# Optimization experiments

Measured on AMD Instinct MI355X. Metric: run time of the kernel, lower is better.

Reference implementation:

```python
import jax, jax.numpy as jnp
import numpy as np

TOP_K = 2

def setup_inputs() -> dict:
    key = jax.random.key(0)
    k1, k2 = jax.random.split(key)
    x = jax.random.normal(k1, (8, 4096, 4096), dtype=jnp.float32)
    # nn.Linear weight [num_experts, dim]
    gate_w = jax.random.normal(k2, (64, 4096), dtype=jnp.float32) * (1.0 / np.sqrt(4096))
    return {"x": x, "gate_w": gate_w}

def reference(x, gate_w):
    # logits: [B, S, E]
    logits = jnp.einsum('bsd,ed->bse', x, gate_w)
    routing_weights = jax.nn.softmax(logits, axis=-1)
    top_weights, top_indices = jax.lax.top_k(routing_weights, TOP_K)
    top_weights = top_weights / jnp.sum(top_weights, axis=-1, keepdims=True)
    return top_weights, top_indices
```

## Files before the change

kernel.cpp:

```cpp
#include <hip/hip_runtime.h>
#include <hip/hip_bf16.h>
#include <math.h>


typedef __attribute__((ext_vector_type(8))) short short8;
typedef __attribute__((ext_vector_type(4))) float f32x4;

#define TPB 64
#define NCH 128
#define TAU 1e-4f
#define LROW 68

__device__ __forceinline__ void cvt8(const f32x4* v, short8* hi, short8* lo) {
    const float* f = reinterpret_cast<const float*>(v);
#pragma unroll
    for (int j = 0; j < 8; ++j) {
        __hip_bfloat16 h = __float2bfloat16(f[j]);
        float r = f[j] - __bfloat162float(h);
        __hip_bfloat16 l = __float2bfloat16(r);
        (*hi)[j] = (short)*reinterpret_cast<unsigned short*>(&h);
        (*lo)[j] = (short)*reinterpret_cast<unsigned short*>(&l);
    }
}

__global__ void prep_b(const float* __restrict__ gw,
                       short8* __restrict__ bh, short8* __restrict__ bl) {
    const int tid = blockIdx.x * 256 + threadIdx.x;
    const int ln  = tid & 63;
    const int w   = (tid >> 6) & 127;
    const int nt  = tid >> 13;
    const int row = nt * 16 + (ln & 15);
    const int k   = w * 32 + ((ln >> 4) << 3);
    f32x4 v[2];
    v[0] = *reinterpret_cast<const f32x4*>(gw + (long)row * 4096 + k);
    v[1] = *reinterpret_cast<const f32x4*>(gw + (long)row * 4096 + k + 4);
    short8 h, l;
    cvt8(v, &h, &l);
    bh[tid] = h;
    bl[tid] = l;
}

__device__ __forceinline__ void gload16(const void* g, void* l) {
    __builtin_amdgcn_global_load_lds(
        (const __attribute__((address_space(1))) void*)g,
        (__attribute__((address_space(3))) void*)l, 16, 0, 0);
}

#define STAGE(C, MBUF) do {                                                   \
    char* aB = AB + (MBUF) * 16384;                                           \
    char* bB = aB + 8192;                                                     \
    _Pragma("unroll")                                                         \
    for (int i = 0; i < 2; ++i)                                               \
        gload16(srcA[i] + (long)(C) * 128, aB + (wv * 2 + i) * 1024 + ln * 16); \
    _Pragma("unroll")                                                         \
    for (int i = 0; i < 2; ++i) {                                             \
        const int s  = wv * 2 + i;                                            \
        const short8* sp = ((s & 1) ? blp : bhp)                              \
            + ((long)(s >> 1) * 8192 + (long)(C) * 64 + ln);                  \
        gload16(sp, bB + s * 1024 + ln * 16);                                 \
    }                                                                         \
} while (0)

__global__ __launch_bounds__(256, 3)
void router_fused(const float* __restrict__ x,
                  const short8* __restrict__ bhp,
                  const short8* __restrict__ blp,
                  const float* __restrict__ gw,
                  float* __restrict__ out,
                  int M, int K) {
    __shared__ __align__(16) char AB[49152];
    __shared__ int flags[TPB];
    __shared__ double Ld4[4][64];

    const int t  = threadIdx.x;
    const int wv = t >> 6;
    const int ln = t & 63;
    const int fr = ln & 15;
    const int q  = ln >> 4;
    const long tok0 = (long)blockIdx.x * TPB;
    const int phase = blockIdx.x & (NCH - 1);

    const char* srcA[2];
#pragma unroll
    for (int i = 0; i < 2; ++i) {
        const int row  = (wv * 2 + i) * 8 + (ln >> 3);
        const int slot = (ln & 7) ^ (row & 7);
        srcA[i] = (const char*)x + (tok0 + row) * (long)K * 4 + slot * 16;
    }

    f32x4 acc[4];
#pragma unroll
    for (int nt = 0; nt < 4; ++nt) acc[nt] = (f32x4){0.f, 0.f, 0.f, 0.f};

    STAGE(phase, 0);
    STAGE((phase + 1) & (NCH - 1), 1);

    const int R  = wv * 16 + fr;
    const int rk = R & 7;

    for (int j = 0; j < NCH; ++j) {
        const int c = (phase + j) & (NCH - 1);
        const int m = j % 3;
        if (j < NCH - 1) asm volatile("s_waitcnt vmcnt(4)" ::: "memory");
        else             asm volatile("s_waitcnt vmcnt(0)" ::: "memory");
        __builtin_amdgcn_s_barrier();
        asm volatile("" ::: "memory");
        if (j + 2 < NCH) STAGE((phase + j + 2) & (NCH - 1), (j + 2) % 3);
        __builtin_amdgcn_sched_barrier(0);

        {
            const char* aB = AB + m * 16384 + R * 128;
            const char* bB = AB + m * 16384 + 8192;
            f32x4 av[2];
            av[0] = *(const f32x4*)(aB + (((q * 2 + 0) ^ rk) * 16));
            av[1] = *(const f32x4*)(aB + (((q * 2 + 1) ^ rk) * 16));
            short8 ah, al;
            cvt8(av, &ah, &al);
            __builtin_amdgcn_s_setprio(1);
#pragma unroll
            for (int nt = 0; nt < 4; ++nt) {
                short8 bhv = *(const short8*)(bB + (nt * 2 + 0) * 1024 + ln * 16);
                short8 blv = *(const short8*)(bB + (nt * 2 + 1) * 1024 + ln * 16);
                acc[nt] = __builtin_amdgcn_mfma_f32_16x16x32_bf16(ah, bhv, acc[nt], 0, 0, 0);
                acc[nt] = __builtin_amdgcn_mfma_f32_16x16x32_bf16(ah, blv, acc[nt], 0, 0, 0);
                acc[nt] = __builtin_amdgcn_mfma_f32_16x16x32_bf16(al, bhv, acc[nt], 0, 0, 0);
                acc[nt] = __builtin_amdgcn_mfma_f32_16x16x32_bf16(al, blv, acc[nt], 0, 0, 0);
            }
            __builtin_amdgcn_s_setprio(0);
        }
        __builtin_amdgcn_sched_barrier(0);
        asm volatile("" ::: "memory");
    }

    __syncthreads();
    float* Ls = (float*)AB;
#pragma unroll
    for (int nt = 0; nt < 4; ++nt)
#pragma unroll
        for (int r = 0; r < 4; ++r)
            Ls[(wv * 16 + q * 4 + r) * LROW + nt * 16 + fr] = acc[nt][r];
    __syncthreads();

    if (t < TPB) {
        const float* row = Ls + (long)t * LROW;
        float m1 = -INFINITY, m2 = -INFINITY, m3 = -INFINITY;
        int i1 = 0, i2 = 0;
#pragma unroll 8
        for (int e = 0; e < 64; ++e) {
            const float v = row[e];
            if (v > m1)      { m3 = m2; m2 = m1; i2 = i1; m1 = v; i1 = e; }
            else if (v > m2) { m3 = m2; m2 = v; i2 = e; }
            else if (v > m3) { m3 = v; }
        }
        const float e2 = expf(m2 - m1);
        const float s  = 1.0f + e2;

        const long g = tok0 + t;
        out[2 * g + 0] = 1.0f / s;
        out[2 * g + 1] = e2 / s;
        float* oi = out + 2 * (long)M;
        oi[2 * g + 0] = (float)i1;
        oi[2 * g + 1] = (float)i2;

        flags[t] = ((m1 - m2) < TAU) | ((m2 - m3) < TAU);
    }
    __syncthreads();

    for (int tk = 0; tk < TPB; ++tk) {
        if (flags[tk]) {
            const float* xr = x + (tok0 + tk) * (long)K + wv * 1024;
            const float* gr = gw + (long)ln * (long)K + wv * 1024;
            double s0 = 0.0, s1 = 0.0, s2 = 0.0, s3 = 0.0;
            for (int k = 0; k < 1024; k += 4) {
                const f32x4 a = *reinterpret_cast<const f32x4*>(xr + k);
                const f32x4 b = *reinterpret_cast<const f32x4*>(gr + k);
                s0 = fma((double)a.x, (double)b.x, s0);
                s1 = fma((double)a.y, (double)b.y, s1);
                s2 = fma((double)a.z, (double)b.z, s2);
                s3 = fma((double)a.w, (double)b.w, s3);
            }
            Ld4[wv][ln] = (s0 + s1) + (s2 + s3);
            __syncthreads();
            if (t == 0) {
                double m1 = -INFINITY, m2 = -INFINITY;
                int i1 = 0, i2 = 0;
                for (int e = 0; e < 64; ++e) {
                    const double v = Ld4[0][e] + Ld4[1][e] + Ld4[2][e] + Ld4[3][e];
                    if (v > m1)      { m2 = m1; i2 = i1; m1 = v; i1 = e; }
                    else if (v > m2) { m2 = v; i2 = e; }
                }
                const double e2 = exp(m2 - m1);
                const double s  = 1.0 + e2;
                const long g = tok0 + tk;
                out[2 * g + 0] = (float)(1.0 / s);
                out[2 * g + 1] = (float)(e2 / s);
                float* oi = out + 2 * (long)M;
                oi[2 * g + 0] = (float)i1;
                oi[2 * g + 1] = (float)i2;
            }
            __syncthreads();
        }
    }
}

extern "C" void kernel_launch(void* const* d_in, const int* in_sizes, int n_in,
                              void* d_out, int out_size, void* d_ws, size_t ws_size,
                              hipStream_t stream) {
    const float* x  = (const float*)d_in[0];
    const float* gw = (const float*)d_in[1];
    float* out = (float*)d_out;

    const int K = 4096;
    const int M = in_sizes[0] / K;
    const int nblocks = M / TPB;

    short8* bh = (short8*)d_ws;
    short8* bl = bh + 32768;

    prep_b<<<128, 256, 0, stream>>>(gw, bh, bl);
    router_fused<<<nblocks, 256, 0, stream>>>(x, bh, bl, gw, out, M, K);
}
```

Before: 246.7 us.

## Double tokens per block and reuse gate-weight tiles across two row tiles

```diff
diff --git a/kernel.cpp b/kernel.cpp
--- a/kernel.cpp
+++ b/kernel.cpp
@@ -6,7 +6,7 @@
 typedef __attribute__((ext_vector_type(8))) short short8;
 typedef __attribute__((ext_vector_type(4))) float f32x4;
 
-#define TPB 64
+#define TPB 128
 #define NCH 128
 #define TAU 1e-4f
 #define LROW 68
@@ -46,12 +46,12 @@
         (__attribute__((address_space(3))) void*)l, 16, 0, 0);
 }
 
-#define STAGE(C, MBUF) do {                                                   \
-    char* aB = AB + (MBUF) * 16384;                                           \
-    char* bB = aB + 8192;                                                     \
+#define STAGE(C, BUF) do {                                                    \
+    char* aB = AB + (BUF) * 24576;                                            \
+    char* bB = aB + 16384;                                                    \
     _Pragma("unroll")                                                         \
-    for (int i = 0; i < 2; ++i)                                               \
-        gload16(srcA[i] + (long)(C) * 128, aB + (wv * 2 + i) * 1024 + ln * 16); \
+    for (int i = 0; i < 4; ++i)                                               \
+        gload16(srcA[i] + (long)(C) * 128, aB + (wv * 4 + i) * 1024 + ln * 16); \
     _Pragma("unroll")                                                         \
     for (int i = 0; i < 2; ++i) {                                             \
         const int s  = wv * 2 + i;                                            \
@@ -80,65 +80,75 @@
     const long tok0 = (long)blockIdx.x * TPB;
     const int phase = blockIdx.x & (NCH - 1);
 
-    const char* srcA[2];
-#pragma unroll
-    for (int i = 0; i < 2; ++i) {
-        const int row  = (wv * 2 + i) * 8 + (ln >> 3);
+    const char* srcA[4];
+#pragma unroll
+    for (int i = 0; i < 4; ++i) {
+        const int row  = (wv * 4 + i) * 8 + (ln >> 3);
         const int slot = (ln & 7) ^ (row & 7);
         srcA[i] = (const char*)x + (tok0 + row) * (long)K * 4 + slot * 16;
     }
 
-    f32x4 acc[4];
-#pragma unroll
-    for (int nt = 0; nt < 4; ++nt) acc[nt] = (f32x4){0.f, 0.f, 0.f, 0.f};
+    f32x4 acc[2][4];
+#pragma unroll
+    for (int i = 0; i < 2; ++i)
+#pragma unroll
+        for (int nt = 0; nt < 4; ++nt) acc[i][nt] = (f32x4){0.f, 0.f, 0.f, 0.f};
 
     STAGE(phase, 0);
     STAGE((phase + 1) & (NCH - 1), 1);
 
-    const int R  = wv * 16 + fr;
-    const int rk = R & 7;
-
     for (int j = 0; j < NCH; ++j) {
-        const int c = (phase + j) & (NCH - 1);
-        const int m = j % 3;
-        if (j < NCH - 1) asm volatile("s_waitcnt vmcnt(4)" ::: "memory");
+        const int c   = (phase + j) & (NCH - 1);
+        const int buf = j & 1;
+        if (j + 1 < NCH) asm volatile("s_waitcnt vmcnt(6)" ::: "memory");
         else             asm volatile("s_waitcnt vmcnt(0)" ::: "memory");
         __builtin_amdgcn_s_barrier();
         asm volatile("" ::: "memory");
-        if (j + 2 < NCH) STAGE((phase + j + 2) & (NCH - 1), (j + 2) % 3);
         __builtin_amdgcn_sched_barrier(0);
+        (void)c;
 
         {
-            const char* aB = AB + m * 16384 + R * 128;
-            const char* bB = AB + m * 16384 + 8192;
-            f32x4 av[2];
-            av[0] = *(const f32x4*)(aB + (((q * 2 + 0) ^ rk) * 16));
-            av[1] = *(const f32x4*)(aB + (((q * 2 + 1) ^ rk) * 16));
-            short8 ah, al;
-            cvt8(av, &ah, &al);
-            __builtin_amdgcn_s_setprio(1);
-#pragma unroll
-            for (int nt = 0; nt < 4; ++nt) {
-                short8 bhv = *(const short8*)(bB + (nt * 2 + 0) * 1024 + ln * 16);
-                short8 blv = *(const short8*)(bB + (nt * 2 + 1) * 1024 + ln * 16);
-                acc[nt] = __builtin_amdgcn_mfma_f32_16x16x32_bf16(ah, bhv, acc[nt], 0, 0, 0);
-                acc[nt] = __builtin_amdgcn_mfma_f32_16x16x32_bf16(ah, blv, acc[nt], 0, 0, 0);
-                acc[nt] = __builtin_amdgcn_mfma_f32_16x16x32_bf16(al, bhv, acc[nt], 0, 0, 0);
-                acc[nt] = __builtin_amdgcn_mfma_f32_16x16x32_bf16(al, blv, acc[nt], 0, 0, 0);
+            const char* aB = AB + buf * 24576;
+            const char* bB = aB + 16384;
+#pragma unroll
+            for (int i = 0; i < 2; ++i) {
+                const int R  = (wv * 2 + i) * 16 + fr;
+                const int rk = R & 7;
+                const char* ar = aB + R * 128;
+                f32x4 av[2];
+                av[0] = *(const f32x4*)(ar + (((q * 2 + 0) ^ rk) * 16));
+                av[1] = *(const f32x4*)(ar + (((q * 2 + 1) ^ rk) * 16));
+                short8 ah, al;
+                cvt8(av, &ah, &al);
+#pragma unroll
+                for (int nt = 0; nt < 4; ++nt) {
+                    short8 bhv = *(const short8*)(bB + (nt * 2 + 0) * 1024 + ln * 16);
+                    short8 blv = *(const short8*)(bB + (nt * 2 + 1) * 1024 + ln * 16);
+                    acc[i][nt] = __builtin_amdgcn_mfma_f32_16x16x32_bf16(ah, bhv, acc[i][nt], 0, 0, 0);
+                    acc[i][nt] = __builtin_amdgcn_mfma_f32_16x16x32_bf16(ah, blv, acc[i][nt], 0, 0, 0);
+                    acc[i][nt] = __builtin_amdgcn_mfma_f32_16x16x32_bf16(al, bhv, acc[i][nt], 0, 0, 0);
+                    acc[i][nt] = __builtin_amdgcn_mfma_f32_16x16x32_bf16(al, blv, acc[i][nt], 0, 0, 0);
+                }
             }
-            __builtin_amdgcn_s_setprio(0);
         }
+
         __builtin_amdgcn_sched_barrier(0);
         asm volatile("" ::: "memory");
+        __builtin_amdgcn_s_barrier();
+        asm volatile("" ::: "memory");
+        if (j + 2 < NCH) STAGE((phase + j + 2) & (NCH - 1), buf);
+        __builtin_amdgcn_sched_barrier(0);
     }
 
     __syncthreads();
     float* Ls = (float*)AB;
 #pragma unroll
-    for (int nt = 0; nt < 4; ++nt)
-#pragma unroll
-        for (int r = 0; r < 4; ++r)
-            Ls[(wv * 16 + q * 4 + r) * LROW + nt * 16 + fr] = acc[nt][r];
+    for (int i = 0; i < 2; ++i)
+#pragma unroll
+        for (int nt = 0; nt < 4; ++nt)
+#pragma unroll
+            for (int r = 0; r < 4; ++r)
+                Ls[((wv * 2 + i) * 16 + q * 4 + r) * LROW + nt * 16 + fr] = acc[i][nt][r];
     __syncthreads();
 
     if (t < TPB) {
```

Result: slower. 264.3 us (+7.1%).
